# Kernel optimization log

Hardware: AMD Instinct MI355X
Metric: run time of the kernel (lower is better)

## Reference

```python
import jax, jax.numpy as jnp
import numpy as np

B, S, D = 2, 2048, 2048
NQ, NKV = 32, 8
HD = D // NQ  # 64
THETA = 10000.0


def _rope_tables(seq_len, head_dim, theta):
    k = jnp.arange(0, head_dim, 2)[: head_dim // 2].astype(jnp.float32)
    inv_freq = 1.0 / (theta ** (k / head_dim))
    pos = jnp.arange(seq_len, dtype=jnp.float32)
    ang = pos[:, None] * inv_freq[None, :]          # [S, HD/2]
    ang = jnp.concatenate([ang, ang], axis=-1)       # [S, HD]
    return jnp.cos(ang), jnp.sin(ang)


def _apply_rope(x, cos, sin):
    # x: [B, H, S, HD]; cos/sin: [S, HD]
    h = x.shape[-1] // 2
    x1, x2 = x[..., :h], x[..., h:]
    rotated = jnp.concatenate([-x2, x1], axis=-1)
    return (x * cos[None, None] + rotated * sin[None, None]).astype(x.dtype)


def setup_inputs() -> dict:
    key = jax.random.key(0)
    ks = jax.random.split(key, 6)
    x = jax.random.normal(ks[0], (B, S, D), dtype=jnp.float32)
    attention_mask = jnp.ones((B, S), dtype=jnp.int32)
    Wq = jax.random.normal(ks[1], (NQ * HD, D), dtype=jnp.float32) * 0.02
    Wk = jax.random.normal(ks[2], (NKV * HD, D), dtype=jnp.float32) * 0.02
    Wv = jax.random.normal(ks[3], (NKV * HD, D), dtype=jnp.float32) * 0.02
    Wo = jax.random.normal(ks[4], (D, D), dtype=jnp.float32) * 0.02
    return {"x": x, "attention_mask": attention_mask,
            "Wq": Wq, "Wk": Wk, "Wv": Wv, "Wo": Wo}


def reference(x, attention_mask, Wq, Wk, Wv, Wo):
    b, s, d = x.shape
    # projections (nn.Linear: y = x @ W.T)
    q = jnp.einsum('bsd,od->bso', x, Wq).reshape(b, s, NQ, HD).transpose(0, 2, 1, 3)
    k = jnp.einsum('bsd,od->bso', x, Wk).reshape(b, s, NKV, HD).transpose(0, 2, 1, 3)
    v = jnp.einsum('bsd,od->bso', x, Wv).reshape(b, s, NKV, HD).transpose(0, 2, 1, 3)
    cos, sin = _rope_tables(s, HD, THETA)
    q = _apply_rope(q, cos, sin)
    k = _apply_rope(k, cos, sin)
    g = NQ // NKV
    k = jnp.repeat(k, g, axis=1)  # [b, NQ, s, HD]
    v = jnp.repeat(v, g, axis=1)
    attn = jnp.einsum('bhqd,bhkd->bhqk', q, k)
    causal = jnp.triu(jnp.ones((s, s), dtype=bool), k=1)
    attn = jnp.where(causal[None, None], -jnp.inf, attn)
    attn = jax.nn.softmax(attn / jnp.sqrt(jnp.float32(HD)), axis=-1)
    out = jnp.einsum('bhqk,bhkd->bhqd', attn, v)
    out = out.transpose(0, 2, 1, 3).reshape(b, s, d)
    return jnp.einsum('bsd,od->bso', out, Wo)
```

## Files before the change

### kernel.cpp

```cpp
#include <hip/hip_runtime.h>

#define B_   2
#define S_   2048
#define D_   2048
#define NQ_  32
#define NKV_ 8
#define HD_  64

typedef unsigned short u16;
typedef __bf16 bf16x8 __attribute__((ext_vector_type(8)));
typedef __bf16 bf16x4 __attribute__((ext_vector_type(4)));
typedef short  s16x4  __attribute__((ext_vector_type(4)));
typedef float  f32x4  __attribute__((ext_vector_type(4)));

#define GLB __attribute__((address_space(1)))
#define LDS __attribute__((address_space(3)))

__device__ inline u16 f2b(float f){
  union { float f; unsigned u; } v; v.f = f;
  unsigned r = (v.u + 0x7fffu + ((v.u >> 16) & 1u)) >> 16;
  return (u16)r;
}

__device__ inline f32x4 mfma16(bf16x4 a, bf16x4 b, f32x4 c){
  union U { bf16x4 b; s16x4 s; };
  U ua, ub; ua.b = a; ub.b = b;
  return __builtin_amdgcn_mfma_f32_16x16x16bf16_1k(ua.s, ub.s, c, 0, 0, 0);
}

__global__ void k_f2b_all(const float* __restrict__ x,  const float* __restrict__ wq,
                          const float* __restrict__ wk, const float* __restrict__ wv,
                          const float* __restrict__ wo,
                          u16* __restrict__ xb, u16* __restrict__ wqkvb, u16* __restrict__ wob){
  int i = blockIdx.x * blockDim.x + threadIdx.x;
  const float* src; u16* dst; int off;
  if (i < 2097152)      { src = x;  dst = xb;                  off = i; }
  else if (i < 3145728) { src = wq; dst = wqkvb;               off = i - 2097152; }
  else if (i < 3407872) { src = wk; dst = wqkvb + 2048*2048;   off = i - 3145728; }
  else if (i < 3670016) { src = wv; dst = wqkvb + 2560*2048;   off = i - 3407872; }
  else                  { src = wo; dst = wob;                 off = i - 3670016; }
  float4 f = ((const float4*)src)[off];
  uint2 pk;
  pk.x = (unsigned)f2b(f.x) | ((unsigned)f2b(f.y) << 16);
  pk.y = (unsigned)f2b(f.z) | ((unsigned)f2b(f.w) << 16);
  ((uint2*)dst)[off] = pk;
}

#define GEMM_CORE(K)                                                           \
  __shared__ __align__(16) u16 As[128*64];                                     \
  __shared__ __align__(16) u16 Bs[128*64];                                     \
  const int tid  = threadIdx.x;                                               \
  const int lane = tid & 63;                                                  \
  const int wave = tid >> 6;                                                  \
  const int wm = wave >> 1, wn = wave & 1;                                    \
  const int quad = lane >> 4, l16 = lane & 15;                                \
  const u16* Ab = A  + (size_t)blockIdx.y * 128 * (K);                        \
  const u16* Bb = Bm + (size_t)blockIdx.x * 128 * (K);                        \
  f32x4 acc[4][4];                                                            \
  for (int i = 0; i < 4; i++)                                                 \
    for (int j = 0; j < 4; j++) acc[i][j] = (f32x4){0.f, 0.f, 0.f, 0.f};      \
  const int R0 = wave * 32;                                                   \
  const int lr = lane >> 3;                                                   \
  const int gc = ((lane & 7) ^ lr) * 8;                                       \
  const int sk = l16 & 7;                                                     \
  for (int k0 = 0; k0 < (K); k0 += 64){                                       \
    __syncthreads();                                                          \
    _Pragma("unroll")                                                         \
    for (int m = 0; m < 4; m++){                                              \
      const u16* ga = Ab + (size_t)(R0 + m*8 + lr) * (K) + k0 + gc;           \
      const u16* gb = Bb + (size_t)(R0 + m*8 + lr) * (K) + k0 + gc;           \
      __builtin_amdgcn_global_load_lds((const GLB void*)ga, (LDS void*)&As[(R0 + m*8)*64], 16, 0, 0); \
      __builtin_amdgcn_global_load_lds((const GLB void*)gb, (LDS void*)&Bs[(R0 + m*8)*64], 16, 0, 0); \
    }                                                                          \
    __syncthreads();                                                          \
    bf16x8 af[4][2], bfr[4][2];                                               \
    _Pragma("unroll")                                                         \
    for (int i = 0; i < 4; i++)                                               \
      _Pragma("unroll")                                                       \
      for (int h = 0; h < 2; h++)                                             \
        af[i][h]  = *(const bf16x8*)&As[(wm*64 + i*16 + l16)*64 + (((h*4 + quad) ^ sk)*8)]; \
    _Pragma("unroll")                                                         \
    for (int j = 0; j < 4; j++)                                               \
      _Pragma("unroll")                                                       \
      for (int h = 0; h < 2; h++)                                             \
        bfr[j][h] = *(const bf16x8*)&Bs[(wn*64 + j*16 + l16)*64 + (((h*4 + quad) ^ sk)*8)]; \
    _Pragma("unroll")                                                         \
    for (int i = 0; i < 4; i++)                                               \
      _Pragma("unroll")                                                       \
      for (int j = 0; j < 4; j++){                                            \
        acc[i][j] = __builtin_amdgcn_mfma_f32_16x16x32_bf16(af[i][0], bfr[j][0], acc[i][j], 0, 0, 0); \
        acc[i][j] = __builtin_amdgcn_mfma_f32_16x16x32_bf16(af[i][1], bfr[j][1], acc[i][j], 0, 0, 0); \
      }                                                                        \
  }

#define QSCALE 0.18033688011112042f
__global__ __launch_bounds__(256) void k_gemm_qkv(const u16* __restrict__ A,
                                                  const u16* __restrict__ Bm,
                                                  u16* __restrict__ qT,
                                                  u16* __restrict__ kT,
                                                  u16* __restrict__ vT){
  GEMM_CORE(2048)

  const int cb = blockIdx.x*128 + wn*64;

  if (cb < 2560){
    const bool isq = (cb < 2048);
    const int hh   = (isq ? cb : (cb - 2048)) >> 6;
    const int NH   = isq ? NQ_ : NKV_;
    u16* base      = isq ? qT : kT;
    const float sc = isq ? QSCALE : 1.0f;
    #pragma unroll
    for (int j = 0; j < 2; j++){
      const int d2 = j*16 + l16;
      const float invf = __expf(-(float)d2 * (9.210340371976184f / 32.0f));
      #pragma unroll
      for (int i = 0; i < 4; i++){
        const int row0 = blockIdx.y*128 + wm*64 + i*16 + quad*4;
        #pragma unroll
        for (int r = 0; r < 4; r++){
          const int row = row0 + r;
          const int s = row & (S_ - 1), b = row >> 11;
          float ang = (float)s * invf;
          float sn, cs;
          sincosf(ang, &sn, &cs);
          const float x1 = acc[i][j][r] * sc, x2 = acc[i][j+2][r] * sc;
          u16* drow = base + ((size_t)(b*NH + hh) * S_ + s) * 64;
          drow[d2]      = f2b(x1*cs - x2*sn);
          drow[d2 + 32] = f2b(x2*cs + x1*sn);
        }
      }
    }
  } else {
    const int fbase = cb - 2560;
    #pragma unroll
    for (int j = 0; j < 4; j++){
      const int f = fbase + j*16 + l16;
      const int kvh = f >> 6, d = f & 63;
      #pragma unroll
      for (int i = 0; i < 4; i++){
        const int row0 = blockIdx.y*128 + wm*64 + i*16 + quad*4;
        const int s0 = row0 & (S_ - 1), b = row0 >> 11;
        uint2 pk;
        pk.x = (unsigned)f2b(acc[i][j][0]) | ((unsigned)f2b(acc[i][j][1]) << 16);
        pk.y = (unsigned)f2b(acc[i][j][2]) | ((unsigned)f2b(acc[i][j][3]) << 16);
        *(uint2*)(vT + ((size_t)(b*NKV_ + kvh) * 64 + d) * S_ + s0) = pk;
      }
    }
  }
}

__global__ __launch_bounds__(256) void k_gemm_bt(const u16* __restrict__ A,
                                                 const u16* __restrict__ Bm,
                                                 float* __restrict__ C,
                                                 int N){
  GEMM_CORE(2048)
  for (int i = 0; i < 4; i++){
    int row0 = blockIdx.y*128 + wm*64 + i*16 + quad*4;
    for (int j = 0; j < 4; j++){
      int col = blockIdx.x*128 + wn*64 + j*16 + l16;
      for (int r = 0; r < 4; r++)
        C[(size_t)(row0 + r) * N + col] = acc[i][j][r];
    }
  }
}

__global__ __launch_bounds__(256) void k_attn(const u16* __restrict__ qT,
                                              const u16* __restrict__ kT,
                                              const u16* __restrict__ vT,
                                              u16* __restrict__ aout){
  __shared__ __align__(16) u16 Ks[2][64*64];
  __shared__ __align__(16) u16 Vs[2][64*64];

  const int bid  = blockIdx.x;
  const int pair = bid & 15;
  const int h    = (bid >> 4) & 31;
  const int b    = bid >> 9;
  const int kvh  = h >> 2;
  const int lane = threadIdx.x & 63, w = threadIdx.x >> 6;
  const int quad = lane >> 4, l16 = lane & 15;

  const u16* Qh = qT + (size_t)(b*NQ_ + h)    * S_ * 64;
  const u16* Kh = kT + (size_t)(b*NKV_ + kvh) * S_ * 64;
  const u16* Vh = vT + (size_t)(b*NKV_ + kvh) * 64 * S_;

  const int rr = lane >> 3;
  const int gg = (lane & 7) ^ rr;
  const int R  = w * 16;

  auto stage = [&](int c, int buf){
    const int kb = c * 64;
    const u16* gk0 = Kh + (size_t)(kb + R + rr)     * 64 + gg*8;
    const u16* gk1 = Kh + (size_t)(kb + R + 8 + rr) * 64 + gg*8;
    const u16* gv0 = Vh + (size_t)(R + rr)     * S_ + kb + gg*8;
    const u16* gv1 = Vh + (size_t)(R + 8 + rr) * S_ + kb + gg*8;
    __builtin_amdgcn_global_load_lds((const GLB void*)gk0, (LDS void*)&Ks[buf][R*64],     16, 0, 0);
    __builtin_amdgcn_global_load_lds((const GLB void*)gk1, (LDS void*)&Ks[buf][(R+8)*64], 16, 0, 0);
    __builtin_amdgcn_global_load_lds((const GLB void*)gv0, (LDS void*)&Vs[buf][R*64],     16, 0, 0);
    __builtin_amdgcn_global_load_lds((const GLB void*)gv1, (LDS void*)&Vs[buf][(R+8)*64], 16, 0, 0);
  };

  const int sw = l16 & 7;

  for (int ph = 0; ph < 2; ph++){
    const int qb    = ph ? (31 - pair) : pair;
    const int qbase = qb*64 + w*16;
    const int qrow  = qbase + l16;

    if (ph == 1) __syncthreads();
    stage(0, 0);

    bf16x8 qf0 = *(const bf16x8*)(Qh + (size_t)qrow*64 + quad*8);
    bf16x8 qf1 = *(const bf16x8*)(Qh + (size_t)qrow*64 + 32 + quad*8);

    f32x4 o[4];
    for (int dt = 0; dt < 4; dt++) o[dt] = (f32x4){0.f, 0.f, 0.f, 0.f};
    float lrow = 0.f;

    for (int c = 0; c <= qb; c++){
      const int buf = c & 1;
      const bool diag = (c == qb);
      const int kbase = c*64;
      __syncthreads();
      if (c < qb) stage(c+1, buf^1);

      bf16x4 pk[4];
      #pragma unroll
      for (int t = 0; t < 4; t++){
        if (diag && t > w){
          pk[t] = (bf16x4){(__bf16)0.f, (__bf16)0.f, (__bf16)0.f, (__bf16)0.f};
          continue;
        }
        const int row = t*16 + l16;
        bf16x8 ka0 = *(const bf16x8*)&Ks[buf][row*64 + (((quad    ) ^ sw)*8)];
        bf16x8 ka1 = *(const bf16x8*)&Ks[buf][row*64 + (((quad + 4) ^ sw)*8)];
        f32x4 z = (f32x4){0.f, 0.f, 0.f, 0.f};
        z = __builtin_amdgcn_mfma_f32_16x16x32_bf16(ka0, qf0, z, 0, 0, 0);
        z = __builtin_amdgcn_mfma_f32_16x16x32_bf16(ka1, qf1, z, 0, 0, 0);
        if (diag && t == w){
          #pragma unroll
          for (int r = 0; r < 4; r++)
            if (kbase + t*16 + quad*4 + r > qrow) z[r] = -1e30f;
        }
        #pragma unroll
        for (int r = 0; r < 4; r++){
          float p = exp2f(z[r]);
          lrow += p;
          pk[t][r] = (__bf16)p;
        }
      }

      #pragma unroll
      for (int dt = 0; dt < 4; dt++){
        const int row = dt*16 + l16;
        #pragma unroll
        for (int t = 0; t < 4; t++){
          if (diag && t > w) continue;
          const int ch = (2*t + (quad >> 1)) ^ sw;
          bf16x4 va = *(const bf16x4*)&Vs[buf][row*64 + ch*8 + (quad & 1)*4];
          o[dt] = mfma16(va, pk[t], o[dt]);
        }
      }
    }

    float lsum = lrow;
    lsum += __shfl_xor(lsum, 16, 64);
    lsum += __shfl_xor(lsum, 32, 64);
    float inv = 1.0f / lsum;

    u16* orow = aout + (size_t)(b*S_ + qrow) * D_ + h*64;
    #pragma unroll
    for (int dt = 0; dt < 4; dt++){
      uint2 pkd;
      u16 e0 = f2b(o[dt][0] * inv), e1 = f2b(o[dt][1] * inv);
      u16 e2 = f2b(o[dt][2] * inv), e3 = f2b(o[dt][3] * inv);
      pkd.x = (unsigned)e0 | ((unsigned)e1 << 16);
      pkd.y = (unsigned)e2 | ((unsigned)e3 << 16);
      *(uint2*)(orow + dt*16 + quad*4) = pkd;
    }
  }
}

extern "C" void kernel_launch(void* const* d_in, const int* in_sizes, int n_in,
                              void* d_out, int out_size, void* d_ws, size_t ws_size,
                              hipStream_t stream){
  const float* x  = (const float*)d_in[0];
  const float* Wq = (const float*)d_in[2];
  const float* Wk = (const float*)d_in[3];
  const float* Wv = (const float*)d_in[4];
  const float* Wo = (const float*)d_in[5];

  char* ws = (char*)d_ws;
  u16* xb    = (u16*)(ws);
  u16* wqkvb = (u16*)(ws + 16777216);
  u16* wob   = (u16*)(ws + 29360128);
  u16* qTp   = (u16*)(ws + 37748736);
  u16* kTp   = (u16*)(ws + 54525952);
  u16* vTp   = (u16*)(ws + 58720256);
  u16* attnOut = xb;

  k_f2b_all<<<dim3(18432), 256, 0, stream>>>(x, Wq, Wk, Wv, Wo, xb, wqkvb, wob);

  k_gemm_qkv<<<dim3(24, 32), 256, 0, stream>>>(xb, wqkvb, qTp, kTp, vTp);

  k_attn<<<dim3(1024), 256, 0, stream>>>(qTp, kTp, vTp, attnOut);

  k_gemm_bt<<<dim3(16, 32), 256, 0, stream>>>(attnOut, wob, (float*)d_out, 2048);
}
```

Measured before the change: 327.6 us.

## Process two query tiles per attention block, add occupancy hints and fast sincos

The attention kernel now gives each block two adjacent 64-row query tiles (128 rows) per phase, so each staged K/V tile in LDS is reused by two sets of Q fragments. This halves the grid and the K/V global traffic, at the cost of more registers for doubled accumulators. The GEMM kernels also get a min-blocks-per-CU launch bound of 3, and RoPE uses __sinf/__cosf in place of sincosf, which may lose accuracy at large angles.

```diff
diff --git a/kernel.cpp b/kernel.cpp
--- a/kernel.cpp
+++ b/kernel.cpp
@@ -94,11 +94,11 @@
   }
 
 #define QSCALE 0.18033688011112042f
-__global__ __launch_bounds__(256) void k_gemm_qkv(const u16* __restrict__ A,
-                                                  const u16* __restrict__ Bm,
-                                                  u16* __restrict__ qT,
-                                                  u16* __restrict__ kT,
-                                                  u16* __restrict__ vT){
+__global__ __launch_bounds__(256, 3) void k_gemm_qkv(const u16* __restrict__ A,
+                                                     const u16* __restrict__ Bm,
+                                                     u16* __restrict__ qT,
+                                                     u16* __restrict__ kT,
+                                                     u16* __restrict__ vT){
   GEMM_CORE(2048)
 
   const int cb = blockIdx.x*128 + wn*64;
@@ -121,8 +121,7 @@
           const int row = row0 + r;
           const int s = row & (S_ - 1), b = row >> 11;
           float ang = (float)s * invf;
-          float sn, cs;
-          sincosf(ang, &sn, &cs);
+          float sn = __sinf(ang), cs = __cosf(ang);
           const float x1 = acc[i][j][r] * sc, x2 = acc[i][j+2][r] * sc;
           u16* drow = base + ((size_t)(b*NH + hh) * S_ + s) * 64;
           drow[d2]      = f2b(x1*cs - x2*sn);
@@ -149,10 +148,10 @@
   }
 }
 
-__global__ __launch_bounds__(256) void k_gemm_bt(const u16* __restrict__ A,
-                                                 const u16* __restrict__ Bm,
-                                                 float* __restrict__ C,
-                                                 int N){
+__global__ __launch_bounds__(256, 3) void k_gemm_bt(const u16* __restrict__ A,
+                                                    const u16* __restrict__ Bm,
+                                                    float* __restrict__ C,
+                                                    int N){
   GEMM_CORE(2048)
   for (int i = 0; i < 4; i++){
     int row0 = blockIdx.y*128 + wm*64 + i*16 + quad*4;
@@ -172,9 +171,9 @@
   __shared__ __align__(16) u16 Vs[2][64*64];
 
   const int bid  = blockIdx.x;
-  const int pair = bid & 15;
-  const int h    = (bid >> 4) & 31;
-  const int b    = bid >> 9;
+  const int tp   = bid & 7;
+  const int h    = (bid >> 3) & 31;
+  const int b    = bid >> 8;
   const int kvh  = h >> 2;
   const int lane = threadIdx.x & 63, w = threadIdx.x >> 6;
   const int quad = lane >> 4, l16 = lane & 15;
@@ -202,50 +201,61 @@
   const int sw = l16 & 7;
 
   for (int ph = 0; ph < 2; ph++){
-    const int qb    = ph ? (31 - pair) : pair;
-    const int qbase = qb*64 + w*16;
-    const int qrow  = qbase + l16;
+    const int T   = ph ? (15 - tp) : tp;
+    const int qb0 = 2*T, qb1 = 2*T + 1;
+    const int qr0 = T*128 + w*16 + l16;
+    const int qr1 = qr0 + 64;
 
     if (ph == 1) __syncthreads();
     stage(0, 0);
 
-    bf16x8 qf0 = *(const bf16x8*)(Qh + (size_t)qrow*64 + quad*8);
-    bf16x8 qf1 = *(const bf16x8*)(Qh + (size_t)qrow*64 + 32 + quad*8);
-
-    f32x4 o[4];
-    for (int dt = 0; dt < 4; dt++) o[dt] = (f32x4){0.f, 0.f, 0.f, 0.f};
-    float lrow = 0.f;
-
-    for (int c = 0; c <= qb; c++){
+    bf16x8 qf[2][2];
+    qf[0][0] = *(const bf16x8*)(Qh + (size_t)qr0*64 + quad*8);
+    qf[0][1] = *(const bf16x8*)(Qh + (size_t)qr0*64 + 32 + quad*8);
+    qf[1][0] = *(const bf16x8*)(Qh + (size_t)qr1*64 + quad*8);
+    qf[1][1] = *(const bf16x8*)(Qh + (size_t)qr1*64 + 32 + quad*8);
+
+    f32x4 o[2][4];
+    #pragma unroll
+    for (int s = 0; s < 2; s++)
+      for (int dt = 0; dt < 4; dt++) o[s][dt] = (f32x4){0.f, 0.f, 0.f, 0.f};
+    float lrow[2] = {0.f, 0.f};
+
+    for (int c = 0; c <= qb1; c++){
       const int buf = c & 1;
-      const bool diag = (c == qb);
-      const int kbase = c*64;
       __syncthreads();
-      if (c < qb) stage(c+1, buf^1);
-
-      bf16x4 pk[4];
+      if (c < qb1) stage(c+1, buf^1);
+
+      const bool act0  = (c <= qb0);
+      const bool diag0 = (c == qb0);
+      const bool diag1 = (c == qb1);
+
+      bf16x4 pk[2][4];
       #pragma unroll
       for (int t = 0; t < 4; t++){
-        if (diag && t > w){
-          pk[t] = (bf16x4){(__bf16)0.f, (__bf16)0.f, (__bf16)0.f, (__bf16)0.f};
-          continue;
-        }
+        const bool n0 = act0 && !(diag0 && t > w);
+        const bool n1 = !(diag1 && t > w);
+        if (!n0 && !n1) continue;
         const int row = t*16 + l16;
         bf16x8 ka0 = *(const bf16x8*)&Ks[buf][row*64 + (((quad    ) ^ sw)*8)];
         bf16x8 ka1 = *(const bf16x8*)&Ks[buf][row*64 + (((quad + 4) ^ sw)*8)];
-        f32x4 z = (f32x4){0.f, 0.f, 0.f, 0.f};
-        z = __builtin_amdgcn_mfma_f32_16x16x32_bf16(ka0, qf0, z, 0, 0, 0);
-        z = __builtin_amdgcn_mfma_f32_16x16x32_bf16(ka1, qf1, z, 0, 0, 0);
-        if (diag && t == w){
+        #pragma unroll
+        for (int s = 0; s < 2; s++){
+          if (s == 0 ? !n0 : !n1) continue;
+          f32x4 z = (f32x4){0.f, 0.f, 0.f, 0.f};
+          z = __builtin_amdgcn_mfma_f32_16x16x32_bf16(ka0, qf[s][0], z, 0, 0, 0);
+          z = __builtin_amdgcn_mfma_f32_16x16x32_bf16(ka1, qf[s][1], z, 0, 0, 0);
+          if ((s == 0 ? diag0 : diag1) && t == w){
+            #pragma unroll
+            for (int r = 0; r < 4; r++)
+              if (quad*4 + r > l16) z[r] = -1e30f;
+          }
           #pragma unroll
-          for (int r = 0; r < 4; r++)
-            if (kbase + t*16 + quad*4 + r > qrow) z[r] = -1e30f;
-        }
-        #pragma unroll
-        for (int r = 0; r < 4; r++){
-          float p = exp2f(z[r]);
-          lrow += p;
-          pk[t][r] = (__bf16)p;
+          for (int r = 0; r < 4; r++){
+            float p = exp2f(z[r]);
+            lrow[s] += p;
+            pk[s][t][r] = (__bf16)p;
+          }
         }
       }
 
@@ -254,28 +264,34 @@
         const int row = dt*16 + l16;
         #pragma unroll
         for (int t = 0; t < 4; t++){
-          if (diag && t > w) continue;
+          const bool n0 = act0 && !(diag0 && t > w);
+          const bool n1 = !(diag1 && t > w);
+          if (!n0 && !n1) continue;
           const int ch = (2*t + (quad >> 1)) ^ sw;
           bf16x4 va = *(const bf16x4*)&Vs[buf][row*64 + ch*8 + (quad & 1)*4];
-          o[dt] = mfma16(va, pk[t], o[dt]);
+          if (n0) o[0][dt] = mfma16(va, pk[0][t], o[0][dt]);
+          if (n1) o[1][dt] = mfma16(va, pk[1][t], o[1][dt]);
         }
       }
     }
 
-    float lsum = lrow;
-    lsum += __shfl_xor(lsum, 16, 64);
-    lsum += __shfl_xor(lsum, 32, 64);
-    float inv = 1.0f / lsum;
-
-    u16* orow = aout + (size_t)(b*S_ + qrow) * D_ + h*64;
     #pragma unroll
-    for (int dt = 0; dt < 4; dt++){
-      uint2 pkd;
-      u16 e0 = f2b(o[dt][0] * inv), e1 = f2b(o[dt][1] * inv);
-      u16 e2 = f2b(o[dt][2] * inv), e3 = f2b(o[dt][3] * inv);
-      pkd.x = (unsigned)e0 | ((unsigned)e1 << 16);
-      pkd.y = (unsigned)e2 | ((unsigned)e3 << 16);
-      *(uint2*)(orow + dt*16 + quad*4) = pkd;
+    for (int s = 0; s < 2; s++){
+      float lsum = lrow[s];
+      lsum += __shfl_xor(lsum, 16, 64);
+      lsum += __shfl_xor(lsum, 32, 64);
+      float inv = 1.0f / lsum;
+      const int qrow = s ? qr1 : qr0;
+      u16* orow = aout + (size_t)(b*S_ + qrow) * D_ + h*64;
+      #pragma unroll
+      for (int dt = 0; dt < 4; dt++){
+        uint2 pkd;
+        u16 e0 = f2b(o[s][dt][0] * inv), e1 = f2b(o[s][dt][1] * inv);
+        u16 e2 = f2b(o[s][dt][2] * inv), e3 = f2b(o[s][dt][3] * inv);
+        pkd.x = (unsigned)e0 | ((unsigned)e1 << 16);
+        pkd.y = (unsigned)e2 | ((unsigned)e3 << 16);
+        *(uint2*)(orow + dt*16 + quad*4) = pkd;
+      }
     }
   }
 }
@@ -302,7 +318,7 @@
 
   k_gemm_qkv<<<dim3(24, 32), 256, 0, stream>>>(xb, wqkvb, qTp, kTp, vTp);
 
-  k_attn<<<dim3(1024), 256, 0, stream>>>(qTp, kTp, vTp, attnOut);
+  k_attn<<<dim3(512), 256, 0, stream>>>(qTp, kTp, vTp, attnOut);
 
   k_gemm_bt<<<dim3(16, 32), 256, 0, stream>>>(attnOut, wob, (float*)d_out, 2048);
 }
```

After: 301.4 us. 8.0% less time.

## Cheapen attention inner loop, use fast sincos and occupancy hints in GEMMs

Applied to the files above, without the earlier changes.

Several micro-optimizations land together. The attention loop precomputes swizzled LDS offsets, simplifies the diagonal mask test, and packs probabilities to bf16 by truncation instead of round-to-nearest conversion. The QKV epilogue swaps sincosf for the fast __sinf/__cosf intrinsics. Both GEMMs gain a launch_bounds minimum-blocks hint of 3. Truncated bf16 and fast trig reduce accuracy slightly, and the occupancy hint may force register spilling.

```diff
diff --git a/kernel.cpp b/kernel.cpp
--- a/kernel.cpp
+++ b/kernel.cpp
@@ -26,6 +26,15 @@
   union U { bf16x4 b; s16x4 s; };
   U ua, ub; ua.b = a; ub.b = b;
   return __builtin_amdgcn_mfma_f32_16x16x16bf16_1k(ua.s, ub.s, c, 0, 0, 0);
+}
+
+__device__ inline bf16x4 pack4(float p0, float p1, float p2, float p3){
+  union { float f; unsigned u; } a, b, c, d;
+  a.f = p0; b.f = p1; c.f = p2; d.f = p3;
+  union { uint2 u; bf16x4 v; } r;
+  r.u.x = (a.u >> 16) | (b.u & 0xffff0000u);
+  r.u.y = (c.u >> 16) | (d.u & 0xffff0000u);
+  return r.v;
 }
 
 __global__ void k_f2b_all(const float* __restrict__ x,  const float* __restrict__ wq,
@@ -94,11 +103,11 @@
   }
 
 #define QSCALE 0.18033688011112042f
-__global__ __launch_bounds__(256) void k_gemm_qkv(const u16* __restrict__ A,
-                                                  const u16* __restrict__ Bm,
-                                                  u16* __restrict__ qT,
-                                                  u16* __restrict__ kT,
-                                                  u16* __restrict__ vT){
+__global__ __launch_bounds__(256, 3) void k_gemm_qkv(const u16* __restrict__ A,
+                                                     const u16* __restrict__ Bm,
+                                                     u16* __restrict__ qT,
+                                                     u16* __restrict__ kT,
+                                                     u16* __restrict__ vT){
   GEMM_CORE(2048)
 
   const int cb = blockIdx.x*128 + wn*64;
@@ -121,8 +130,7 @@
           const int row = row0 + r;
           const int s = row & (S_ - 1), b = row >> 11;
           float ang = (float)s * invf;
-          float sn, cs;
-          sincosf(ang, &sn, &cs);
+          float sn = __sinf(ang), cs = __cosf(ang);
           const float x1 = acc[i][j][r] * sc, x2 = acc[i][j+2][r] * sc;
           u16* drow = base + ((size_t)(b*NH + hh) * S_ + s) * 64;
           drow[d2]      = f2b(x1*cs - x2*sn);
@@ -149,10 +157,10 @@
   }
 }
 
-__global__ __launch_bounds__(256) void k_gemm_bt(const u16* __restrict__ A,
-                                                 const u16* __restrict__ Bm,
-                                                 float* __restrict__ C,
-                                                 int N){
+__global__ __launch_bounds__(256, 3) void k_gemm_bt(const u16* __restrict__ A,
+                                                    const u16* __restrict__ Bm,
+                                                    float* __restrict__ C,
+                                                    int N){
   GEMM_CORE(2048)
   for (int i = 0; i < 4; i++){
     int row0 = blockIdx.y*128 + wm*64 + i*16 + quad*4;
@@ -199,12 +207,17 @@
     __builtin_amdgcn_global_load_lds((const GLB void*)gv1, (LDS void*)&Vs[buf][(R+8)*64], 16, 0, 0);
   };
 
-  const int sw = l16 & 7;
+  const int sw    = l16 & 7;
+  const int koff0 = ((quad    ) ^ sw) * 8;
+  const int koff1 = ((quad + 4) ^ sw) * 8;
+  int voff[4];
+  #pragma unroll
+  for (int t = 0; t < 4; t++)
+    voff[t] = (((2*t + (quad >> 1)) ^ sw) * 8) + (quad & 1)*4;
 
   for (int ph = 0; ph < 2; ph++){
-    const int qb    = ph ? (31 - pair) : pair;
-    const int qbase = qb*64 + w*16;
-    const int qrow  = qbase + l16;
+    const int qb   = ph ? (31 - pair) : pair;
+    const int qrow = qb*64 + w*16 + l16;
 
     if (ph == 1) __syncthreads();
     stage(0, 0);
@@ -213,50 +226,47 @@
     bf16x8 qf1 = *(const bf16x8*)(Qh + (size_t)qrow*64 + 32 + quad*8);
 
     f32x4 o[4];
+    #pragma unroll
     for (int dt = 0; dt < 4; dt++) o[dt] = (f32x4){0.f, 0.f, 0.f, 0.f};
     float lrow = 0.f;
 
     for (int c = 0; c <= qb; c++){
       const int buf = c & 1;
       const bool diag = (c == qb);
-      const int kbase = c*64;
       __syncthreads();
       if (c < qb) stage(c+1, buf^1);
+
+      const u16* Kb = &Ks[buf][0];
+      const u16* Vb = &Vs[buf][0];
 
       bf16x4 pk[4];
       #pragma unroll
       for (int t = 0; t < 4; t++){
-        if (diag && t > w){
-          pk[t] = (bf16x4){(__bf16)0.f, (__bf16)0.f, (__bf16)0.f, (__bf16)0.f};
-          continue;
-        }
-        const int row = t*16 + l16;
-        bf16x8 ka0 = *(const bf16x8*)&Ks[buf][row*64 + (((quad    ) ^ sw)*8)];
-        bf16x8 ka1 = *(const bf16x8*)&Ks[buf][row*64 + (((quad + 4) ^ sw)*8)];
+        if (diag && t > w) continue;
+        const int rowb = (t*16 + l16)*64;
+        bf16x8 ka0 = *(const bf16x8*)&Kb[rowb + koff0];
+        bf16x8 ka1 = *(const bf16x8*)&Kb[rowb + koff1];
         f32x4 z = (f32x4){0.f, 0.f, 0.f, 0.f};
         z = __builtin_amdgcn_mfma_f32_16x16x32_bf16(ka0, qf0, z, 0, 0, 0);
         z = __builtin_amdgcn_mfma_f32_16x16x32_bf16(ka1, qf1, z, 0, 0, 0);
         if (diag && t == w){
           #pragma unroll
           for (int r = 0; r < 4; r++)
-            if (kbase + t*16 + quad*4 + r > qrow) z[r] = -1e30f;
+            if (quad*4 + r > l16) z[r] = -1e30f;
         }
-        #pragma unroll
-        for (int r = 0; r < 4; r++){
-          float p = exp2f(z[r]);
-          lrow += p;
-          pk[t][r] = (__bf16)p;
-        }
+        float p0 = exp2f(z[0]), p1 = exp2f(z[1]);
+        float p2 = exp2f(z[2]), p3 = exp2f(z[3]);
+        lrow += (p0 + p1) + (p2 + p3);
+        pk[t] = pack4(p0, p1, p2, p3);
       }
 
       #pragma unroll
       for (int dt = 0; dt < 4; dt++){
-        const int row = dt*16 + l16;
+        const int rowb = (dt*16 + l16)*64;
         #pragma unroll
         for (int t = 0; t < 4; t++){
           if (diag && t > w) continue;
-          const int ch = (2*t + (quad >> 1)) ^ sw;
-          bf16x4 va = *(const bf16x4*)&Vs[buf][row*64 + ch*8 + (quad & 1)*4];
+          bf16x4 va = *(const bf16x4*)&Vb[rowb + voff[t]];
           o[dt] = mfma16(va, pk[t], o[dt]);
         }
       }
```

New measurement: 308.0 us. -6.0%, faster.
